# Performance work log

Measured on AMD Instinct MI355X. Metric: run time of the kernel, lower is better.

Reference implementation:

```python
import jax, jax.numpy as jnp
import numpy as np


def _radial_bins(H, W, d):
    """Radial frequency bin labels (H,W) int32 and one-hot (H*W, nbins) float32.
    label = ceil(min(floor(r), R) / d), R = min(H//2, W//2), r measured from the
    fftshift-ed center, exactly as the torch double loop."""
    ch, cw = H // 2, W // 2
    R = min(ch, cw)
    hh = (jnp.arange(H) - ch).astype(jnp.float32)
    ww = (jnp.arange(W) - cw).astype(jnp.float32)
    r = jnp.sqrt(hh[:, None] ** 2 + ww[None, :] ** 2)
    rf = jnp.minimum(jnp.floor(r), float(R))
    lab = jnp.ceil(rf / d).astype(jnp.int32)  # (H, W), values in [0, R//d]
    nbins = int(R // d) + 1
    onehot = jax.nn.one_hot(lab.reshape(-1), nbins, dtype=jnp.float32)  # (HW, nbins)
    return lab, onehot


def reference(feature, gamma, fc_w, fc_b, group, d):
    B, C, H, W = feature.shape
    K = C // group
    fg = feature.reshape(B, group, K, H, W)
    # ChannelPool(['avg','max']): sum of channel-mean and channel-max -> (B, g, H, W)
    comp = jnp.mean(fg, axis=2) + jnp.max(fg, axis=2)

    spec = jnp.fft.fftshift(jnp.fft.fft2(comp), axes=(-2, -1))
    amp = jnp.abs(spec)          # (B, g, H, W)
    phase = jnp.angle(spec)

    lab, onehot = _radial_bins(H, W, d)
    counts = onehot.sum(axis=0)  # (nbins,)
    # segment mean of amplitude over radial bins
    sums = jnp.einsum('bgp,pn->bgn', amp.reshape(B, group, H * W), onehot)
    pooled = sums / counts       # (B, g, nbins)

    # per-group Linear(ch, ch) + LeakyReLU (torch default slope 0.01)
    att = jax.nn.leaky_relu(jnp.einsum('bgn,gmn->bgm', pooled, fc_w) + fc_b[None], 0.01)

    # scatter gate back to every pixel of its radial bin
    attn_px = att[:, :, lab]     # (B, g, H, W)
    amp1 = amp * attn_px

    merged = jnp.exp(1j * phase) * amp1
    out = jnp.fft.ifft2(jnp.fft.ifftshift(merged, axes=(-2, -1)))
    nf = jnp.real(out)           # (B, g, H, W)

    # global min-max per (b, g) map to [0, 1]
    mn = jnp.min(nf, axis=(-2, -1), keepdims=True)
    mx = jnp.max(nf, axis=(-2, -1), keepdims=True)
    attn_map = (nf - mn) / (mx - mn)

    feature1 = (fg * attn_map[:, :, None]).reshape(B, C, H, W)
    return feature + gamma[None, :, None, None] * feature1


def setup_inputs() -> dict:
    key = jax.random.key(0)
    k1, k2, k3, k4 = jax.random.split(key, 4)
    B, C, H, W = 32, 256, 56, 56
    group, d = 4, 1
    ch = (min(H // 2, W // 2) // d) + 1  # 29
    return {
        'feature': jax.random.normal(k1, (B, C, H, W), dtype=jnp.float32),
        'gamma': jax.random.normal(k2, (C,), dtype=jnp.float32) * 0.1,
        'fc_w': jax.random.normal(k3, (group, ch, ch), dtype=jnp.float32) / np.sqrt(ch),
        'fc_b': jax.random.normal(k4, (group, ch), dtype=jnp.float32) * 0.01,
        'group': group,
        'd': d,
    }
```

## Files before the change

kernel.cpp:

```cpp
#include <hip/hip_runtime.h>
#include <math.h>

constexpr int B_  = 32;
constexpr int C_  = 256;
constexpr int G_  = 4;
constexpr int K_  = 64;
constexpr int P_  = 3136;
constexpr int NB_ = 29;
constexpr int BG_ = 128;
constexpr int CP_ = C_ * P_;
constexpr int N_  = B_ * CP_;
constexpr int N4_ = N_ / 4;
constexpr float TWO_PI = 6.283185307179586f;

typedef float f4_t __attribute__((ext_vector_type(4)));

__device__ __forceinline__ int lab_of(int p) {
    int h = p / 56, w = p - h * 56;
    int hh = ((h + 28) % 56) - 28;
    int ww = ((w + 28) % 56) - 28;
    int r2 = hh * hh + ww * ww;
    int rf = (int)sqrtf((float)r2);
    while ((rf + 1) * (rf + 1) <= r2) ++rf;
    while (rf * rf > r2) --rf;
    if (rf > 28) rf = 28;
    return rf;
}

__device__ __forceinline__ unsigned fkey(float f) {
    unsigned u = __float_as_uint(f);
    return (u & 0x80000000u) ? ~u : (u | 0x80000000u);
}
__device__ __forceinline__ float fdec(unsigned k) {
    return (k & 0x80000000u) ? __uint_as_float(k ^ 0x80000000u) : __uint_as_float(~k);
}


__global__ __launch_bounds__(256) void comp_f1_kernel(const float* __restrict__ feature,
                                                      float2* __restrict__ tmpF,
                                                      float* __restrict__ sums,
                                                      unsigned* __restrict__ mnmx) {
    int blk = blockIdx.x, bg = blk / 14, rblk = blk - bg * 14, r0 = rblk * 4;
    int b = bg >> 2, g = bg & 3;
    int t = threadIdx.x;
    __shared__ float  sx[4][57];
    __shared__ float2 stw[56];
    if (rblk == 0) {
        if (t < NB_) sums[bg * NB_ + t] = 0.f;
        else if (t == NB_)     mnmx[bg * 2]     = 0xFFFFFFFFu;
        else if (t == NB_ + 1) mnmx[bg * 2 + 1] = 0u;
    }
    if (t < 56) { float a = -TWO_PI * (float)t / 56.f; stw[t] = make_float2(cosf(a), sinf(a)); }
    if (t < 224) {
        const float* base = feature + (b * C_ + g * K_) * P_ + r0 * 56 + t;
        float sum = 0.f, mx = -INFINITY;
#pragma unroll 8
        for (int k = 0; k < K_; ++k) {
            float v = base[k * P_];
            sum += v;
            mx = fmaxf(mx, v);
        }
        sx[t / 56][t % 56] = sum * (1.f / 64.f) + mx;
    }
    __syncthreads();
    if (t < 224) {
        int r = t & 3, k = t >> 2;
        float sr = 0.f, si = 0.f; int idx = 0;
        for (int j = 0; j < 56; ++j) {
            float v = sx[r][j];
            float2 tw = stw[idx];
            sr = fmaf(v, tw.x, sr); si = fmaf(v, tw.y, si);
            idx += k; if (idx >= 56) idx -= 56;
        }
        tmpF[bg * P_ + k * 56 + (r0 + r)] = make_float2(sr, si);
    }
}

__global__ __launch_bounds__(256) void f2_kernel(const float2* __restrict__ tmpF,
                                                 float2* __restrict__ specS,
                                                 float* __restrict__ sums,
                                                 float* __restrict__ inv_cnt) {
    int blk = blockIdx.x, bg = blk / 14, r0 = (blk - bg * 14) * 4;
    __shared__ float2 sx[4][57];
    __shared__ float2 sT[4][57];
    __shared__ float2 w56[56];
    __shared__ float2 w8[8];
    __shared__ float  sbins[NB_];
    int t = threadIdx.x;
    if (t < 56) { float a = -TWO_PI * (float)t / 56.f; w56[t] = make_float2(cosf(a), sinf(a)); }
    if (t < 8)  { float a = -TWO_PI * (float)t / 8.f;  w8[t]  = make_float2(cosf(a), sinf(a)); }
    if (t < NB_) sbins[t] = 0.f;
    if (t < 224) sx[t / 56][t % 56] = tmpF[bg * P_ + (r0 + t / 56) * 56 + (t % 56)];
    __syncthreads();
    if (t < 224) {
        int r = t / 56, j = t - r * 56;
        int n1 = j >> 3, k0 = j & 7;
        float sr = 0.f, si = 0.f; int i8 = 0;
        for (int n2 = 0; n2 < 8; ++n2) {
            float2 a = sx[r][7 * n2 + n1];
            float2 w = w8[i8];
            sr = fmaf(a.x, w.x, fmaf(-a.y, w.y, sr));
            si = fmaf(a.x, w.y, fmaf( a.y, w.x, si));
            i8 = (i8 + k0) & 7;
        }
        sT[r][j] = make_float2(sr, si);
    }
    __syncthreads();
    if (t < 224) {
        int r = t / 56, k = t - r * 56;
        float sr = 0.f, si = 0.f; int idx = 0;
        for (int n1 = 0; n1 < 7; ++n1) {
            float2 a = sT[r][(n1 << 3) + (k & 7)];
            float2 w = w56[idx];
            sr = fmaf(a.x, w.x, fmaf(-a.y, w.y, sr));
            si = fmaf(a.x, w.y, fmaf( a.y, w.x, si));
            idx += k; if (idx >= 56) idx -= 56;
        }
        specS[bg * P_ + (r0 + r) * 56 + k] = make_float2(sr, si);
        float amp = sqrtf(sr * sr + si * si);
        atomicAdd(&sbins[lab_of(k * 56 + (r0 + r))], amp);
    }
    __syncthreads();
    if (t < NB_) atomicAdd(&sums[bg * NB_ + t], sbins[t]);
    if (blk == 0) {
        __shared__ int s_cnt[NB_];
        if (t < NB_) s_cnt[t] = 0;
        __syncthreads();
        for (int p = t; p < P_; p += 256) atomicAdd(&s_cnt[lab_of(p)], 1);
        __syncthreads();
        if (t < NB_) inv_cnt[t] = 1.0f / (float)s_cnt[t];
    }
}

__global__ __launch_bounds__(256) void i1fc_kernel(const float2* __restrict__ specS,
                                                   const float* __restrict__ sums,
                                                   const float* __restrict__ inv_cnt,
                                                   const float* __restrict__ fc_w,
                                                   const float* __restrict__ fc_b,
                                                   float2* __restrict__ A_s) {
    int blk = blockIdx.x, bg = blk / 14, r0 = (blk - bg * 14) * 4;
    int g = bg & 3;
    __shared__ float2 sx[4][57];
    __shared__ float2 sT[4][57];
    __shared__ float2 w56[56];
    __shared__ float2 w8[8];
    __shared__ float  s_pool[NB_], s_att[NB_];
    int t = threadIdx.x;
    if (t < 56) { float a = TWO_PI * (float)t / 56.f; w56[t] = make_float2(cosf(a), sinf(a)); }
    if (t < 8)  { float a = TWO_PI * (float)t / 8.f;  w8[t]  = make_float2(cosf(a), sinf(a)); }
    if (t < NB_) s_pool[t] = sums[bg * NB_ + t] * inv_cnt[t];
    __syncthreads();
    if (t < NB_) {
        float acc = fc_b[g * NB_ + t];
        const float* wrow = &fc_w[(g * NB_ + t) * NB_];
        for (int n = 0; n < NB_; ++n) acc = fmaf(s_pool[n], wrow[n], acc);
        s_att[t] = acc >= 0.f ? acc : 0.01f * acc;
    }
    __syncthreads();
    if (t < 224) {
        int r = t / 56, kh = t - r * 56;
        int kw = r0 + r;
        float2 v = specS[bg * P_ + kw * 56 + kh];
        float a = s_att[lab_of(kh * 56 + kw)];
        sx[r][kh] = make_float2(v.x * a, v.y * a);
    }
    __syncthreads();
    if (t < 224) {
        int r = t / 56, j = t - r * 56;
        int n1 = j >> 3, k0 = j & 7;
        float sr = 0.f, si = 0.f; int i8 = 0;
        for (int n2 = 0; n2 < 8; ++n2) {
            float2 a = sx[r][7 * n2 + n1];
            float2 w = w8[i8];
            sr = fmaf(a.x, w.x, fmaf(-a.y, w.y, sr));
            si = fmaf(a.x, w.y, fmaf( a.y, w.x, si));
            i8 = (i8 + k0) & 7;
        }
        sT[r][j] = make_float2(sr, si);
    }
    __syncthreads();
    if (t < 224) {
        int r = t / 56, h = t - r * 56;
        float sr = 0.f, si = 0.f; int idx = 0;
        for (int n1 = 0; n1 < 7; ++n1) {
            float2 a = sT[r][(n1 << 3) + (h & 7)];
            float2 w = w56[idx];
            sr = fmaf(a.x, w.x, fmaf(-a.y, w.y, sr));
            si = fmaf(a.x, w.y, fmaf( a.y, w.x, si));
            idx += h; if (idx >= 56) idx -= 56;
        }
        A_s[bg * P_ + h * 56 + (r0 + r)] = make_float2(sr, si);
    }
}

__global__ __launch_bounds__(256) void i2_kernel(const float2* __restrict__ A_s,
                                                 float* __restrict__ nf,
                                                 unsigned* __restrict__ mnmx) {
    int blk = blockIdx.x, bg = blk / 14, h0 = (blk - bg * 14) * 4;
    __shared__ float2 sx[4][57];
    __shared__ float2 sT[4][57];
    __shared__ float2 w56[56];
    __shared__ float2 w8[8];
    __shared__ float  red_mn[256], red_mx[256];
    int t = threadIdx.x;
    if (t < 56) { float a = TWO_PI * (float)t / 56.f; w56[t] = make_float2(cosf(a), sinf(a)); }
    if (t < 8)  { float a = TWO_PI * (float)t / 8.f;  w8[t]  = make_float2(cosf(a), sinf(a)); }
    if (t < 224) sx[t / 56][t % 56] = A_s[bg * P_ + (h0 + t / 56) * 56 + (t % 56)];
    __syncthreads();
    if (t < 224) {
        int r = t / 56, j = t - r * 56;
        int n1 = j >> 3, k0 = j & 7;
        float sr = 0.f, si = 0.f; int i8 = 0;
        for (int n2 = 0; n2 < 8; ++n2) {
            float2 a = sx[r][7 * n2 + n1];
            float2 w = w8[i8];
            sr = fmaf(a.x, w.x, fmaf(-a.y, w.y, sr));
            si = fmaf(a.x, w.y, fmaf( a.y, w.x, si));
            i8 = (i8 + k0) & 7;
        }
        sT[r][j] = make_float2(sr, si);
    }
    __syncthreads();
    float lmn = INFINITY, lmx = -INFINITY;
    if (t < 224) {
        int r = t / 56, w = t - r * 56;
        float sr = 0.f; int idx = 0;
        for (int n1 = 0; n1 < 7; ++n1) {
            float2 a = sT[r][(n1 << 3) + (w & 7)];
            float2 tw = w56[idx];
            sr = fmaf(a.x, tw.x, fmaf(-a.y, tw.y, sr));
            idx += w; if (idx >= 56) idx -= 56;
        }
        float v = sr * (1.0f / (float)P_);
        nf[bg * P_ + (h0 + r) * 56 + w] = v;
        lmn = v; lmx = v;
    }
    red_mn[t] = lmn; red_mx[t] = lmx;
    __syncthreads();
    for (int off = 128; off > 0; off >>= 1) {
        if (t < off) {
            red_mn[t] = fminf(red_mn[t], red_mn[t + off]);
            red_mx[t] = fmaxf(red_mx[t], red_mx[t + off]);
        }
        __syncthreads();
    }
    if (t == 0) {
        atomicMin(&mnmx[bg * 2 + 0], fkey(red_mn[0]));
        atomicMax(&mnmx[bg * 2 + 1], fkey(red_mx[0]));
    }
}

__global__ __launch_bounds__(256) void final_kernel(const float* __restrict__ feature,
                                                    const float* __restrict__ gamma,
                                                    const float* __restrict__ nf,
                                                    const unsigned* __restrict__ mnmx,
                                                    float* __restrict__ out) {
    int i = blockIdx.x * 256 + threadIdx.x;
    int b = i / (C_ * 784);
    int rem = i - b * (C_ * 784);
    int c = rem / 784;
    int p4 = rem - c * 784;
    int bg = (b << 2) | (c >> 6);
    float mn = fdec(mnmx[bg * 2 + 0]);
    float mx = fdec(mnmx[bg * 2 + 1]);
    float inv = 1.0f / (mx - mn);
    float4 f = ((const float4*)feature)[i];
    float4 v = ((const float4*)nf)[bg * 784 + p4];
    float gam = gamma[c];
    f4_t o;
    o.x = f.x + gam * f.x * ((v.x - mn) * inv);
    o.y = f.y + gam * f.y * ((v.y - mn) * inv);
    o.z = f.z + gam * f.z * ((v.z - mn) * inv);
    o.w = f.w + gam * f.w * ((v.w - mn) * inv);
    __builtin_nontemporal_store(o, ((f4_t*)out) + i);
}

extern "C" void kernel_launch(void* const* d_in, const int* in_sizes, int n_in,
                              void* d_out, int out_size, void* d_ws, size_t ws_size,
                              hipStream_t stream) {
    const float* feature = (const float*)d_in[0];
    const float* gamma   = (const float*)d_in[1];
    const float* fc_w    = (const float*)d_in[2];
    const float* fc_b    = (const float*)d_in[3];

    float* ws = (float*)d_ws;
    float2*   tmpF    = (float2*)ws;
    float2*   specS   = (float2*)(ws + 802816);
    float*    nf      = ws + 1605632;
    float*    sums    = ws + 2007040;
    float*    inv_cnt = ws + 2010752;
    unsigned* mnmx    = (unsigned*)(ws + 2010784);
    float2*   A_s     = tmpF;
    float*    out     = (float*)d_out;

    comp_f1_kernel<<<BG_ * 14, 256, 0, stream>>>(feature, tmpF, sums, mnmx);
    f2_kernel     <<<BG_ * 14, 256, 0, stream>>>(tmpF, specS, sums, inv_cnt);
    i1fc_kernel   <<<BG_ * 14, 256, 0, stream>>>(specS, sums, inv_cnt, fc_w, fc_b, A_s);
    i2_kernel     <<<BG_ * 14, 256, 0, stream>>>(A_s, nf, mnmx);
    final_kernel  <<<N4_ / 256, 256, 0, stream>>>(feature, gamma, nf, mnmx, out);
}
```

Before: 77.92 us.

## Fuse inverse FFT passes using Hermitian symmetry of gated spectrum

The forward FFT now stores only the non-redundant half of the spectrum (29 of 56 columns), since the input is real and the gate is radially symmetric. The two inverse-FFT kernels are merged into one: each block loads the half spectrum, computes only its 4 output rows of the column DFT, and then does a real-output row transform that uses conjugate symmetry. This removes one kernel launch and the full complex intermediate round trip through global memory. In exchange, each block repeats the gating and first-stage DFT for all 29 columns, and the redundant DFT work is spread across the 14 blocks of each map.

```diff
diff --git a/kernel.cpp b/kernel.cpp
--- a/kernel.cpp
+++ b/kernel.cpp
@@ -108,6 +108,7 @@
     __syncthreads();
     if (t < 224) {
         int r = t / 56, k = t - r * 56;
+        int kw = r0 + r;
         float sr = 0.f, si = 0.f; int idx = 0;
         for (int n1 = 0; n1 < 7; ++n1) {
             float2 a = sT[r][(n1 << 3) + (k & 7)];
@@ -116,9 +117,9 @@
             si = fmaf(a.x, w.y, fmaf( a.y, w.x, si));
             idx += k; if (idx >= 56) idx -= 56;
         }
-        specS[bg * P_ + (r0 + r) * 56 + k] = make_float2(sr, si);
+        if (kw <= 28) specS[bg * 29 * 56 + kw * 56 + k] = make_float2(sr, si);
         float amp = sqrtf(sr * sr + si * si);
-        atomicAdd(&sbins[lab_of(k * 56 + (r0 + r))], amp);
+        atomicAdd(&sbins[lab_of(k * 56 + kw)], amp);
     }
     __syncthreads();
     if (t < NB_) atomicAdd(&sums[bg * NB_ + t], sbins[t]);
@@ -132,19 +133,22 @@
     }
 }
 
-__global__ __launch_bounds__(256) void i1fc_kernel(const float2* __restrict__ specS,
-                                                   const float* __restrict__ sums,
-                                                   const float* __restrict__ inv_cnt,
-                                                   const float* __restrict__ fc_w,
-                                                   const float* __restrict__ fc_b,
-                                                   float2* __restrict__ A_s) {
-    int blk = blockIdx.x, bg = blk / 14, r0 = (blk - bg * 14) * 4;
+__global__ __launch_bounds__(256) void i12fc_kernel(const float2* __restrict__ specS,
+                                                    const float* __restrict__ sums,
+                                                    const float* __restrict__ inv_cnt,
+                                                    const float* __restrict__ fc_w,
+                                                    const float* __restrict__ fc_b,
+                                                    float* __restrict__ nf,
+                                                    unsigned* __restrict__ mnmx) {
+    int blk = blockIdx.x, bg = blk / 14, h0 = (blk - bg * 14) * 4;
     int g = bg & 3;
-    __shared__ float2 sx[4][57];
-    __shared__ float2 sT[4][57];
+    __shared__ float2 s_spec[29][57];
+    __shared__ float2 sT[29][29];
+    __shared__ float2 sA[4][30];
     __shared__ float2 w56[56];
     __shared__ float2 w8[8];
     __shared__ float  s_pool[NB_], s_att[NB_];
+    __shared__ float  red_mn[256], red_mx[256];
     int t = threadIdx.x;
     if (t < 56) { float a = TWO_PI * (float)t / 56.f; w56[t] = make_float2(cosf(a), sinf(a)); }
     if (t < 8)  { float a = TWO_PI * (float)t / 8.f;  w8[t]  = make_float2(cosf(a), sinf(a)); }
@@ -157,81 +161,54 @@
         s_att[t] = acc >= 0.f ? acc : 0.01f * acc;
     }
     __syncthreads();
-    if (t < 224) {
-        int r = t / 56, kh = t - r * 56;
-        int kw = r0 + r;
-        float2 v = specS[bg * P_ + kw * 56 + kh];
+    for (int i = t; i < 29 * 56; i += 256) {
+        int kw = i / 56, kh = i - kw * 56;
+        float2 v = specS[bg * 29 * 56 + i];
         float a = s_att[lab_of(kh * 56 + kw)];
-        sx[r][kh] = make_float2(v.x * a, v.y * a);
-    }
-    __syncthreads();
-    if (t < 224) {
-        int r = t / 56, j = t - r * 56;
-        int n1 = j >> 3, k0 = j & 7;
+        s_spec[kw][kh] = make_float2(v.x * a, v.y * a);
+    }
+    __syncthreads();
+    for (int i = t; i < 29 * 28; i += 256) {
+        int kw = i / 28, j = i - kw * 28;
+        int n1 = j >> 2, r = j & 3;
+        int k0 = (h0 + r) & 7;
         float sr = 0.f, si = 0.f; int i8 = 0;
         for (int n2 = 0; n2 < 8; ++n2) {
-            float2 a = sx[r][7 * n2 + n1];
+            float2 a = s_spec[kw][7 * n2 + n1];
             float2 w = w8[i8];
             sr = fmaf(a.x, w.x, fmaf(-a.y, w.y, sr));
             si = fmaf(a.x, w.y, fmaf( a.y, w.x, si));
             i8 = (i8 + k0) & 7;
         }
-        sT[r][j] = make_float2(sr, si);
-    }
-    __syncthreads();
-    if (t < 224) {
-        int r = t / 56, h = t - r * 56;
+        sT[kw][(n1 << 2) + r] = make_float2(sr, si);
+    }
+    __syncthreads();
+    if (t < 116) {
+        int r = t / 29, kw = t - r * 29;
+        int h = h0 + r;
         float sr = 0.f, si = 0.f; int idx = 0;
         for (int n1 = 0; n1 < 7; ++n1) {
-            float2 a = sT[r][(n1 << 3) + (h & 7)];
+            float2 a = sT[kw][(n1 << 2) + r];
             float2 w = w56[idx];
             sr = fmaf(a.x, w.x, fmaf(-a.y, w.y, sr));
             si = fmaf(a.x, w.y, fmaf( a.y, w.x, si));
             idx += h; if (idx >= 56) idx -= 56;
         }
-        A_s[bg * P_ + h * 56 + (r0 + r)] = make_float2(sr, si);
-    }
-}
-
-__global__ __launch_bounds__(256) void i2_kernel(const float2* __restrict__ A_s,
-                                                 float* __restrict__ nf,
-                                                 unsigned* __restrict__ mnmx) {
-    int blk = blockIdx.x, bg = blk / 14, h0 = (blk - bg * 14) * 4;
-    __shared__ float2 sx[4][57];
-    __shared__ float2 sT[4][57];
-    __shared__ float2 w56[56];
-    __shared__ float2 w8[8];
-    __shared__ float  red_mn[256], red_mx[256];
-    int t = threadIdx.x;
-    if (t < 56) { float a = TWO_PI * (float)t / 56.f; w56[t] = make_float2(cosf(a), sinf(a)); }
-    if (t < 8)  { float a = TWO_PI * (float)t / 8.f;  w8[t]  = make_float2(cosf(a), sinf(a)); }
-    if (t < 224) sx[t / 56][t % 56] = A_s[bg * P_ + (h0 + t / 56) * 56 + (t % 56)];
-    __syncthreads();
-    if (t < 224) {
-        int r = t / 56, j = t - r * 56;
-        int n1 = j >> 3, k0 = j & 7;
-        float sr = 0.f, si = 0.f; int i8 = 0;
-        for (int n2 = 0; n2 < 8; ++n2) {
-            float2 a = sx[r][7 * n2 + n1];
-            float2 w = w8[i8];
-            sr = fmaf(a.x, w.x, fmaf(-a.y, w.y, sr));
-            si = fmaf(a.x, w.y, fmaf( a.y, w.x, si));
-            i8 = (i8 + k0) & 7;
-        }
-        sT[r][j] = make_float2(sr, si);
+        sA[r][kw] = make_float2(sr, si);
     }
     __syncthreads();
     float lmn = INFINITY, lmx = -INFINITY;
     if (t < 224) {
         int r = t / 56, w = t - r * 56;
-        float sr = 0.f; int idx = 0;
-        for (int n1 = 0; n1 < 7; ++n1) {
-            float2 a = sT[r][(n1 << 3) + (w & 7)];
+        float acc = sA[r][0].x + ((w & 1) ? -sA[r][28].x : sA[r][28].x);
+        int idx = w;
+        for (int kw = 1; kw < 28; ++kw) {
+            float2 a = sA[r][kw];
             float2 tw = w56[idx];
-            sr = fmaf(a.x, tw.x, fmaf(-a.y, tw.y, sr));
+            acc = fmaf(2.f * a.x, tw.x, fmaf(-2.f * a.y, tw.y, acc));
             idx += w; if (idx >= 56) idx -= 56;
         }
-        float v = sr * (1.0f / (float)P_);
+        float v = acc * (1.0f / (float)P_);
         nf[bg * P_ + (h0 + r) * 56 + w] = v;
         lmn = v; lmx = v;
     }
@@ -286,16 +263,14 @@
     float* ws = (float*)d_ws;
     float2*   tmpF    = (float2*)ws;
     float2*   specS   = (float2*)(ws + 802816);
-    float*    nf      = ws + 1605632;
-    float*    sums    = ws + 2007040;
-    float*    inv_cnt = ws + 2010752;
-    unsigned* mnmx    = (unsigned*)(ws + 2010784);
-    float2*   A_s     = tmpF;
+    float*    nf      = ws + 1218560;
+    float*    sums    = ws + 1619968;
+    float*    inv_cnt = ws + 1623680;
+    unsigned* mnmx    = (unsigned*)(ws + 1623712);
     float*    out     = (float*)d_out;
 
     comp_f1_kernel<<<BG_ * 14, 256, 0, stream>>>(feature, tmpF, sums, mnmx);
     f2_kernel     <<<BG_ * 14, 256, 0, stream>>>(tmpF, specS, sums, inv_cnt);
-    i1fc_kernel   <<<BG_ * 14, 256, 0, stream>>>(specS, sums, inv_cnt, fc_w, fc_b, A_s);
-    i2_kernel     <<<BG_ * 14, 256, 0, stream>>>(A_s, nf, mnmx);
+    i12fc_kernel  <<<BG_ * 14, 256, 0, stream>>>(specS, sums, inv_cnt, fc_w, fc_b, nf, mnmx);
     final_kernel  <<<N4_ / 256, 256, 0, stream>>>(feature, gamma, nf, mnmx, out);
 }
```

New measurement: 82.99 us. 1.07x slower.

## Exploit Hermitian symmetry of real-input FFT to halve spectral work

Applied to the files above, without the earlier changes.

Uses the conjugate symmetry of the 2D FFT of the real pooled map to compute and store only 29 of the 56 frequency columns. The column DFT, spectral gating and first inverse pass all work on half the columns, with mirrored amplitudes given weight 2 in the radial-bin sums. The last inverse pass rebuilds the missing half by conjugation. This cuts FFT arithmetic and workspace traffic in the middle kernels, but those kernels are small next to the full-tensor read and write passes, and the 29-column blocks leave some threads idle.

```diff
diff --git a/kernel.cpp b/kernel.cpp
--- a/kernel.cpp
+++ b/kernel.cpp
@@ -11,6 +11,7 @@
 constexpr int CP_ = C_ * P_;
 constexpr int N_  = B_ * CP_;
 constexpr int N4_ = N_ / 4;
+constexpr int HP_ = 29 * 56;
 constexpr float TWO_PI = 6.283185307179586f;
 
 typedef float f4_t __attribute__((ext_vector_type(4)));
@@ -63,7 +64,7 @@
         sx[t / 56][t % 56] = sum * (1.f / 64.f) + mx;
     }
     __syncthreads();
-    if (t < 224) {
+    if (t < 116) {
         int r = t & 3, k = t >> 2;
         float sr = 0.f, si = 0.f; int idx = 0;
         for (int j = 0; j < 56; ++j) {
@@ -72,7 +73,7 @@
             sr = fmaf(v, tw.x, sr); si = fmaf(v, tw.y, si);
             idx += k; if (idx >= 56) idx -= 56;
         }
-        tmpF[bg * P_ + k * 56 + (r0 + r)] = make_float2(sr, si);
+        tmpF[bg * HP_ + k * 56 + (r0 + r)] = make_float2(sr, si);
     }
 }
 
@@ -80,7 +81,7 @@
                                                  float2* __restrict__ specS,
                                                  float* __restrict__ sums,
                                                  float* __restrict__ inv_cnt) {
-    int blk = blockIdx.x, bg = blk / 14, r0 = (blk - bg * 14) * 4;
+    int blk = blockIdx.x, bg = blk >> 3, kw0 = (blk & 7) * 4;
     __shared__ float2 sx[4][57];
     __shared__ float2 sT[4][57];
     __shared__ float2 w56[56];
@@ -90,7 +91,10 @@
     if (t < 56) { float a = -TWO_PI * (float)t / 56.f; w56[t] = make_float2(cosf(a), sinf(a)); }
     if (t < 8)  { float a = -TWO_PI * (float)t / 8.f;  w8[t]  = make_float2(cosf(a), sinf(a)); }
     if (t < NB_) sbins[t] = 0.f;
-    if (t < 224) sx[t / 56][t % 56] = tmpF[bg * P_ + (r0 + t / 56) * 56 + (t % 56)];
+    if (t < 224) {
+        int r = t / 56, c = t - r * 56;
+        if (kw0 + r <= 28) sx[r][c] = tmpF[bg * HP_ + (kw0 + r) * 56 + c];
+    }
     __syncthreads();
     if (t < 224) {
         int r = t / 56, j = t - r * 56;
@@ -108,17 +112,21 @@
     __syncthreads();
     if (t < 224) {
         int r = t / 56, k = t - r * 56;
-        float sr = 0.f, si = 0.f; int idx = 0;
-        for (int n1 = 0; n1 < 7; ++n1) {
-            float2 a = sT[r][(n1 << 3) + (k & 7)];
-            float2 w = w56[idx];
-            sr = fmaf(a.x, w.x, fmaf(-a.y, w.y, sr));
-            si = fmaf(a.x, w.y, fmaf( a.y, w.x, si));
-            idx += k; if (idx >= 56) idx -= 56;
-        }
-        specS[bg * P_ + (r0 + r) * 56 + k] = make_float2(sr, si);
-        float amp = sqrtf(sr * sr + si * si);
-        atomicAdd(&sbins[lab_of(k * 56 + (r0 + r))], amp);
+        int kw = kw0 + r;
+        if (kw <= 28) {
+            float sr = 0.f, si = 0.f; int idx = 0;
+            for (int n1 = 0; n1 < 7; ++n1) {
+                float2 a = sT[r][(n1 << 3) + (k & 7)];
+                float2 w = w56[idx];
+                sr = fmaf(a.x, w.x, fmaf(-a.y, w.y, sr));
+                si = fmaf(a.x, w.y, fmaf( a.y, w.x, si));
+                idx += k; if (idx >= 56) idx -= 56;
+            }
+            specS[bg * HP_ + kw * 56 + k] = make_float2(sr, si);
+            float amp = sqrtf(sr * sr + si * si);
+            float wgt = (kw == 0 || kw == 28) ? 1.f : 2.f;
+            atomicAdd(&sbins[lab_of(k * 56 + kw)], amp * wgt);
+        }
     }
     __syncthreads();
     if (t < NB_) atomicAdd(&sums[bg * NB_ + t], sbins[t]);
@@ -138,7 +146,7 @@
                                                    const float* __restrict__ fc_w,
                                                    const float* __restrict__ fc_b,
                                                    float2* __restrict__ A_s) {
-    int blk = blockIdx.x, bg = blk / 14, r0 = (blk - bg * 14) * 4;
+    int blk = blockIdx.x, bg = blk >> 3, kw0 = (blk & 7) * 4;
     int g = bg & 3;
     __shared__ float2 sx[4][57];
     __shared__ float2 sT[4][57];
@@ -159,10 +167,12 @@
     __syncthreads();
     if (t < 224) {
         int r = t / 56, kh = t - r * 56;
-        int kw = r0 + r;
-        float2 v = specS[bg * P_ + kw * 56 + kh];
-        float a = s_att[lab_of(kh * 56 + kw)];
-        sx[r][kh] = make_float2(v.x * a, v.y * a);
+        int kw = kw0 + r;
+        if (kw <= 28) {
+            float2 v = specS[bg * HP_ + kw * 56 + kh];
+            float a = s_att[lab_of(kh * 56 + kw)];
+            sx[r][kh] = make_float2(v.x * a, v.y * a);
+        }
     }
     __syncthreads();
     if (t < 224) {
@@ -181,15 +191,18 @@
     __syncthreads();
     if (t < 224) {
         int r = t / 56, h = t - r * 56;
-        float sr = 0.f, si = 0.f; int idx = 0;
-        for (int n1 = 0; n1 < 7; ++n1) {
-            float2 a = sT[r][(n1 << 3) + (h & 7)];
-            float2 w = w56[idx];
-            sr = fmaf(a.x, w.x, fmaf(-a.y, w.y, sr));
-            si = fmaf(a.x, w.y, fmaf( a.y, w.x, si));
-            idx += h; if (idx >= 56) idx -= 56;
-        }
-        A_s[bg * P_ + h * 56 + (r0 + r)] = make_float2(sr, si);
+        int kw = kw0 + r;
+        if (kw <= 28) {
+            float sr = 0.f, si = 0.f; int idx = 0;
+            for (int n1 = 0; n1 < 7; ++n1) {
+                float2 a = sT[r][(n1 << 3) + (h & 7)];
+                float2 w = w56[idx];
+                sr = fmaf(a.x, w.x, fmaf(-a.y, w.y, sr));
+                si = fmaf(a.x, w.y, fmaf( a.y, w.x, si));
+                idx += h; if (idx >= 56) idx -= 56;
+            }
+            A_s[bg * HP_ + h * 29 + kw] = make_float2(sr, si);
+        }
     }
 }
 
@@ -205,7 +218,12 @@
     int t = threadIdx.x;
     if (t < 56) { float a = TWO_PI * (float)t / 56.f; w56[t] = make_float2(cosf(a), sinf(a)); }
     if (t < 8)  { float a = TWO_PI * (float)t / 8.f;  w8[t]  = make_float2(cosf(a), sinf(a)); }
-    if (t < 224) sx[t / 56][t % 56] = A_s[bg * P_ + (h0 + t / 56) * 56 + (t % 56)];
+    if (t < 116) {
+        int r = t / 29, kw = t - r * 29;
+        float2 v = A_s[bg * HP_ + (h0 + r) * 29 + kw];
+        sx[r][kw] = v;
+        if (kw >= 1 && kw <= 27) sx[r][56 - kw] = make_float2(v.x, -v.y);
+    }
     __syncthreads();
     if (t < 224) {
         int r = t / 56, j = t - r * 56;
@@ -285,17 +303,17 @@
 
     float* ws = (float*)d_ws;
     float2*   tmpF    = (float2*)ws;
-    float2*   specS   = (float2*)(ws + 802816);
-    float*    nf      = ws + 1605632;
-    float*    sums    = ws + 2007040;
-    float*    inv_cnt = ws + 2010752;
-    unsigned* mnmx    = (unsigned*)(ws + 2010784);
+    float2*   specS   = (float2*)(ws + 415744);
+    float*    nf      = ws + 831488;
+    float*    sums    = ws + 1232896;
+    float*    inv_cnt = ws + 1236608;
+    unsigned* mnmx    = (unsigned*)(ws + 1236640);
     float2*   A_s     = tmpF;
     float*    out     = (float*)d_out;
 
     comp_f1_kernel<<<BG_ * 14, 256, 0, stream>>>(feature, tmpF, sums, mnmx);
-    f2_kernel     <<<BG_ * 14, 256, 0, stream>>>(tmpF, specS, sums, inv_cnt);
-    i1fc_kernel   <<<BG_ * 14, 256, 0, stream>>>(specS, sums, inv_cnt, fc_w, fc_b, A_s);
+    f2_kernel     <<<BG_ * 8, 256, 0, stream>>>(tmpF, specS, sums, inv_cnt);
+    i1fc_kernel   <<<BG_ * 8, 256, 0, stream>>>(specS, sums, inv_cnt, fc_w, fc_b, A_s);
     i2_kernel     <<<BG_ * 14, 256, 0, stream>>>(A_s, nf, mnmx);
     final_kernel  <<<N4_ / 256, 256, 0, stream>>>(feature, gamma, nf, mnmx, out);
 }
```

Result: faster. 73.41 us (-5.8%).
